# Optimization experiments

Hardware: AMD Instinct MI355X
Metric: run time of the kernel (lower is better)

## Reference

```python
import jax, jax.numpy as jnp
import numpy as np

N_NODES = 100000
N_EDGES = 1600000
D_IN = 128
D_OUT = 128


def setup_inputs() -> dict:
    key = jax.random.key(0)
    k1, k2, k3, k4, k5 = jax.random.split(key, 5)
    features = jax.random.normal(k1, (N_NODES, D_IN), dtype=jnp.float32)
    edge_row = jax.random.randint(k2, (N_EDGES,), 0, N_NODES, dtype=jnp.int32)
    edge_col = jax.random.randint(k3, (N_EDGES,), 0, N_NODES, dtype=jnp.int32)
    edge_val = jax.random.uniform(k4, (N_EDGES,), dtype=jnp.float32)
    # Xavier-uniform weight, zero bias, ones skip weight (matches reset_parameters)
    limit = float(np.sqrt(6.0 / (D_IN + D_OUT)))
    weight = jax.random.uniform(k5, (D_IN, D_OUT), minval=-limit, maxval=limit, dtype=jnp.float32)
    bias = jnp.zeros((D_OUT,), dtype=jnp.float32)
    skip_weight = jnp.ones((D_OUT,), dtype=jnp.float32)
    return {"features": features, "edge_row": edge_row, "edge_col": edge_col,
            "edge_val": edge_val, "weight": weight, "bias": bias,
            "skip_weight": skip_weight}


def reference(features, edge_row, edge_col, edge_val, weight, bias, skip_weight):
    # Dense projection: [N, Din] @ [Din, Dout] -> [N, Dout]
    h = features @ weight
    # SpMM in COO form: Ah[r] = sum_e val[e] * h[col[e]] for edges with row[e]==r
    gathered = edge_val[:, None] * h[edge_col]          # [E, Dout]
    Ah = jax.ops.segment_sum(gathered, edge_row, num_segments=N_NODES)
    # Skip-scale + bias + activation epilogue
    out = h * skip_weight[None, :] + Ah + bias[None, :]
    return jax.nn.selu(out)
```

## Files before the change

kernel.cpp:

```cpp
#include <hip/hip_runtime.h>

#define N_NODES 100000
#define N_EDGES 1600000
#define D 128
#define BM 64
#define GEMM_BLKS 1563

#define BROWS 128
#define NB 782
#define EB 250
#define EPB 6400
#define NTAB (NB * EB)
#define SCAN_BLKS 191

typedef __attribute__((ext_vector_type(8))) short short8_t;
typedef __attribute__((ext_vector_type(4))) float float4_t;

__device__ __forceinline__ unsigned pack_bf16x2(float a, float b) {
    unsigned ua = __float_as_uint(a);
    unsigned ub = __float_as_uint(b);
    ua = (ua + 0x7fffu + ((ua >> 16) & 1u)) >> 16;
    ub = (ub + 0x7fffu + ((ub >> 16) & 1u)) & 0xffff0000u;
    return ua | ub;
}

__device__ __forceinline__ float selu_f(float x) {
    const float SCALE = 1.0507009873554805f;
    const float ALPHA = 1.6732632423543772f;
    return x > 0.f ? SCALE * x : SCALE * ALPHA * (expf(x) - 1.f);
}

__global__ __launch_bounds__(256) void bhist_prep_kernel(
    const int* __restrict__ erow, const float* __restrict__ W,
    unsigned* __restrict__ tbl, unsigned short* __restrict__ wt)
{
    __shared__ unsigned hcnt[NB];
    const int t = threadIdx.x;
    if (blockIdx.x < EB) {
        const int k = blockIdx.x;
        for (int i = t; i < NB; i += 256) hcnt[i] = 0;
        __syncthreads();
        const int4* q = (const int4*)(erow + k * EPB);
        for (int i = t; i < EPB / 4; i += 256) {
            const int4 r = q[i];
            atomicAdd(&hcnt[r.x >> 7], 1u);
            atomicAdd(&hcnt[r.y >> 7], 1u);
            atomicAdd(&hcnt[r.z >> 7], 1u);
            atomicAdd(&hcnt[r.w >> 7], 1u);
        }
        __syncthreads();
        for (int i = t; i < NB; i += 256) tbl[k * NB + i] = hcnt[i];
    } else {
        const int pb = blockIdx.x - EB;
        for (int idx = pb * 4096 + t; idx < (pb + 1) * 4096; idx += 256) {
            const int k = idx >> 7, n = idx & 127;
            unsigned u = __float_as_uint(W[idx]);
            u = (u + 0x7fffu + ((u >> 16) & 1u)) >> 16;
            wt[n * D + k] = (unsigned short)u;
        }
    }
}

__global__ __launch_bounds__(1024) void scan_local_kernel(
    const unsigned* __restrict__ tbl, unsigned* __restrict__ lex,
    unsigned* __restrict__ bsum)
{
    __shared__ unsigned wsum[16];
    const int t = threadIdx.x;
    const int L = blockIdx.x * 1024 + t;
    const int lane = t & 63;

    unsigned v = 0;
    if (L < NTAB) {
        const int b = L / EB;
        const int k = L - b * EB;
        v = tbl[k * NB + b];
    }
    unsigned x = v;
#pragma unroll
    for (int d = 1; d < 64; d <<= 1) {
        const unsigned y = __shfl_up(x, d, 64);
        if (lane >= d) x += y;
    }
    if (lane == 63) wsum[t >> 6] = x;
    __syncthreads();
    unsigned add = 0;
    for (int w = 0; w < (t >> 6); ++w) add += wsum[w];
    x += add;
    if (L < NTAB) lex[L] = x - v;
    if (t == 1023) bsum[blockIdx.x] = x;
}

__global__ __launch_bounds__(256) void scan_blk_kernel(unsigned* __restrict__ bsum)
{
    __shared__ unsigned ws[4];
    const int t = threadIdx.x, lane = t & 63, w = t >> 6;
    unsigned v = (t < SCAN_BLKS) ? bsum[t] : 0u;
    unsigned x = v;
#pragma unroll
    for (int d = 1; d < 64; d <<= 1) {
        const unsigned y = __shfl_up(x, d, 64);
        if (lane >= d) x += y;
    }
    if (lane == 63) ws[w] = x;
    __syncthreads();
    unsigned add = 0;
    for (int i = 0; i < w; ++i) add += ws[i];
    x += add;
    if (t < SCAN_BLKS) bsum[t] = x - v;
}

__global__ __launch_bounds__(1024) void scan_apply_kernel(
    const unsigned* __restrict__ lex, const unsigned* __restrict__ boff,
    unsigned* __restrict__ tbl)
{
    const int L = blockIdx.x * 1024 + threadIdx.x;
    if (L >= NTAB) return;
    const int b = L / EB;
    const int k = L - b * EB;
    tbl[k * NB + b] = lex[L] + boff[blockIdx.x];
}

__global__ __launch_bounds__(256) void gemm_scatter_kernel(
    const float* __restrict__ feat, const unsigned short* __restrict__ wt,
    unsigned* __restrict__ h16,
    const int* __restrict__ erow, const int* __restrict__ ecol,
    const float* __restrict__ eval_, const unsigned* __restrict__ tbl,
    int2* __restrict__ rec)
{
    __shared__ __align__(16) char smem[52224];
    const int t = threadIdx.x;

    if (blockIdx.x < GEMM_BLKS) {
        short* At = (short*)smem;
        short* Wt = (short*)(smem + 17408);
        const int rowBase = blockIdx.x * BM;

        {
            const int n = t >> 1, hf = t & 1;
            const uint4* src = (const uint4*)(wt + n * D + hf * 64);
            uint4* dst = (uint4*)&Wt[n * 136 + hf * 64];
#pragma unroll
            for (int j = 0; j < 8; ++j) dst[j] = src[j];
        }
        {
#pragma unroll
            for (int i = 0; i < 8; ++i) {
                const int p = t + 256 * i;
                const int r = p >> 5, kq = p & 31;
                int row = rowBase + r;
                if (row >= N_NODES) row = N_NODES - 1;
                const float4 f = *(const float4*)&feat[(size_t)row * D + kq * 4];
                uint2 u;
                u.x = pack_bf16x2(f.x, f.y);
                u.y = pack_bf16x2(f.z, f.w);
                *(uint2*)&At[r * 136 + kq * 4] = u;
            }
        }
        __syncthreads();

        const int w = t >> 6, lane = t & 63;
        const int m16 = lane & 15, kg = lane >> 4;

        short8_t a_frag[4];
        const int arow = w * 16 + m16;
#pragma unroll
        for (int k0 = 0; k0 < 4; ++k0)
            a_frag[k0] = *(const short8_t*)&At[arow * 136 + k0 * 32 + kg * 8];

#pragma unroll
        for (int nt = 0; nt < 8; ++nt) {
            float4_t acc = {0.f, 0.f, 0.f, 0.f};
#pragma unroll
            for (int k0 = 0; k0 < 4; ++k0) {
                const short8_t b =
                    *(const short8_t*)&Wt[(nt * 16 + m16) * 136 + k0 * 32 + kg * 8];
                acc = __builtin_amdgcn_mfma_f32_16x16x32_bf16(a_frag[k0], b, acc, 0, 0, 0);
            }
            float mine[4], part[4];
#pragma unroll
            for (int i = 0; i < 4; ++i) {
                mine[i] = acc[i];
                part[i] = __shfl_xor(mine[i], 1, 64);
            }
            if ((m16 & 1) == 0) {
                const int cp = (nt * 16 + m16) >> 1;
#pragma unroll
                for (int i = 0; i < 4; ++i) {
                    const int row = rowBase + w * 16 + kg * 4 + i;
                    if (row < N_NODES)
                        h16[(size_t)row * 64 + cp] = pack_bf16x2(mine[i], part[i]);
                }
            }
        }
    } else {
        unsigned* rk = (unsigned*)smem;
        const int k = blockIdx.x - GEMM_BLKS;
        for (int i = t; i < NB; i += 256) rk[i] = 0;
        __syncthreads();

        const int4*   qr = (const int4*)(erow + k * EPB);
        const int4*   qc = (const int4*)(ecol + k * EPB);
        const float4* qv = (const float4*)(eval_ + k * EPB);
        const unsigned* base = tbl + k * NB;

        for (int i = t; i < EPB / 4; i += 256) {
            const int4   r = qr[i];
            const int4   c = qc[i];
            const float4 v = qv[i];
            {
                const int b = r.x >> 7;
                const unsigned pos = base[b] + atomicAdd(&rk[b], 1u);
                rec[pos] = make_int2(c.x | ((r.x & 127) << 17), __float_as_int(v.x));
            }
            {
                const int b = r.y >> 7;
                const unsigned pos = base[b] + atomicAdd(&rk[b], 1u);
                rec[pos] = make_int2(c.y | ((r.y & 127) << 17), __float_as_int(v.y));
            }
            {
                const int b = r.z >> 7;
                const unsigned pos = base[b] + atomicAdd(&rk[b], 1u);
                rec[pos] = make_int2(c.z | ((r.z & 127) << 17), __float_as_int(v.z));
            }
            {
                const int b = r.w >> 7;
                const unsigned pos = base[b] + atomicAdd(&rk[b], 1u);
                rec[pos] = make_int2(c.w | ((r.w & 127) << 17), __float_as_int(v.w));
            }
        }
    }
}

__global__ __launch_bounds__(256) void bsort_kernel(
    const unsigned* __restrict__ tbl, const int2* __restrict__ rec,
    int2* __restrict__ rec2, unsigned* __restrict__ rstart)
{
    __shared__ unsigned cnt[BROWS], base[BROWS], rk[BROWS];
    __shared__ unsigned w0tot;
    const int t = threadIdx.x, b = blockIdx.x;
    if (t < BROWS) { cnt[t] = 0; rk[t] = 0; }
    __syncthreads();

    const unsigned s = tbl[b];
    const unsigned e = (b == NB - 1) ? N_EDGES : tbl[b + 1];

    for (unsigned j = s + t; j < e; j += 256)
        atomicAdd(&cnt[(rec[j].x >> 17) & 127], 1u);
    __syncthreads();

    unsigned v = 0, x = 0;
    if (t < BROWS) {
        v = cnt[t]; x = v;
#pragma unroll
        for (int d = 1; d < 64; d <<= 1) {
            const unsigned y = __shfl_up(x, d, 64);
            if ((t & 63) >= d) x += y;
        }
    }
    if (t == 63) w0tot = x;
    __syncthreads();
    if (t < BROWS) {
        const unsigned ex = x - v + ((t >= 64) ? w0tot : 0u);
        base[t] = s + ex;
        const int row = b * BROWS + t;
        if (row < N_NODES) rstart[row] = s + ex;
    }
    __syncthreads();

    for (unsigned j = s + t; j < e; j += 256) {
        const int2 R = rec[j];
        const int rl = (R.x >> 17) & 127;
        const unsigned pos = base[rl] + atomicAdd(&rk[rl], 1u);
        rec2[pos] = R;
    }
}

__global__ __launch_bounds__(256) void spmm_csr_kernel(
    const unsigned* __restrict__ rstart, const int2* __restrict__ rec,
    const unsigned* __restrict__ h16, const float* __restrict__ skip,
    const float* __restrict__ bias, float* __restrict__ out)
{
    const int row = blockIdx.x * 4 + (threadIdx.x >> 6);
    if (row >= N_NODES) return;
    const int lane = threadIdx.x & 63;
    const int half = lane >> 5, sub = lane & 31;

    const unsigned s = rstart[row];
    const unsigned e = (row == N_NODES - 1) ? N_EDGES : rstart[row + 1];

    const uint2* h2 = (const uint2*)h16;

    float4 a0 = make_float4(0.f, 0.f, 0.f, 0.f);
    float4 a1 = a0, a2 = a0, a3 = a0;

    for (unsigned j = s; j < e; j += 16) {
        int2  R[8];
        uint2 p[8];
        float v[8];
#pragma unroll
        for (int k = 0; k < 8; ++k) {
            const unsigned jj = j + 2 * k + half;
            const unsigned ji = jj < e ? jj : e - 1;
            R[k] = rec[ji];
            v[k] = (jj < e) ? __int_as_float(R[k].y) : 0.f;
        }
#pragma unroll
        for (int k = 0; k < 8; ++k)
            p[k] = h2[(size_t)(R[k].x & 0x1FFFF) * 32 + sub];

#pragma unroll
        for (int k = 0; k < 8; ++k) {
            float4* a = (k & 3) == 0 ? &a0 : (k & 3) == 1 ? &a1 : (k & 3) == 2 ? &a2 : &a3;
            a->x += v[k] * __uint_as_float(p[k].x << 16);
            a->y += v[k] * __uint_as_float(p[k].x & 0xffff0000u);
            a->z += v[k] * __uint_as_float(p[k].y << 16);
            a->w += v[k] * __uint_as_float(p[k].y & 0xffff0000u);
        }
    }

    float4 a;
    a.x = (a0.x + a1.x) + (a2.x + a3.x);
    a.y = (a0.y + a1.y) + (a2.y + a3.y);
    a.z = (a0.z + a1.z) + (a2.z + a3.z);
    a.w = (a0.w + a1.w) + (a2.w + a3.w);
    a.x += __shfl_xor(a.x, 32, 64);
    a.y += __shfl_xor(a.y, 32, 64);
    a.z += __shfl_xor(a.z, 32, 64);
    a.w += __shfl_xor(a.w, 32, 64);

    if (half == 0) {
        const int c4 = sub * 4;
        const uint2 hp = h2[(size_t)row * 32 + sub];
        const float4 sk = *(const float4*)&skip[c4];
        const float4 bs = *(const float4*)&bias[c4];
        float4 o;
        o.x = __uint_as_float(hp.x << 16) * sk.x + bs.x + a.x;
        o.y = __uint_as_float(hp.x & 0xffff0000u) * sk.y + bs.y + a.y;
        o.z = __uint_as_float(hp.y << 16) * sk.z + bs.z + a.z;
        o.w = __uint_as_float(hp.y & 0xffff0000u) * sk.w + bs.w + a.w;
        o.x = selu_f(o.x); o.y = selu_f(o.y); o.z = selu_f(o.z); o.w = selu_f(o.w);
        *(float4*)&out[(size_t)row * D + c4] = o;
    }
}

__global__ __launch_bounds__(256) void gemm_fb_kernel(
    const float* __restrict__ feat, const float* __restrict__ W,
    const float* __restrict__ bias, const float* __restrict__ skip,
    float* __restrict__ h, float* __restrict__ out)
{
    __shared__ float Wl[D * D];
    __shared__ float Fl[32 * D];
    const int tid = threadIdx.x;

    const float4* W4 = (const float4*)W;
    float4* Wl4 = (float4*)Wl;
#pragma unroll
    for (int i = 0; i < 16; ++i) Wl4[tid + 256 * i] = W4[tid + 256 * i];

    const size_t rowBase = (size_t)blockIdx.x * 32;
    const float4* F4 = (const float4*)(feat + rowBase * D);
    float4* Fl4 = (float4*)Fl;
#pragma unroll
    for (int i = 0; i < 4; ++i) Fl4[tid + 256 * i] = F4[tid + 256 * i];
    __syncthreads();

    const int colg = (tid & 31) * 4;
    const int row0 = (tid >> 5) * 4;
    float4 acc[4];
#pragma unroll
    for (int r = 0; r < 4; ++r) acc[r] = make_float4(0.f, 0.f, 0.f, 0.f);
#pragma unroll 4
    for (int k = 0; k < D; ++k) {
        const float4 w = *(const float4*)&Wl[k * D + colg];
#pragma unroll
        for (int r = 0; r < 4; ++r) {
            const float aa = Fl[(row0 + r) * D + k];
            acc[r].x += aa * w.x; acc[r].y += aa * w.y;
            acc[r].z += aa * w.z; acc[r].w += aa * w.w;
        }
    }
    const float4 sk = *(const float4*)&skip[colg];
    const float4 bs = *(const float4*)&bias[colg];
#pragma unroll
    for (int r = 0; r < 4; ++r) {
        const size_t row = rowBase + row0 + r;
        *(float4*)&h[row * D + colg] = acc[r];
        float4 o;
        o.x = acc[r].x * sk.x + bs.x; o.y = acc[r].y * sk.y + bs.y;
        o.z = acc[r].z * sk.z + bs.z; o.w = acc[r].w * sk.w + bs.w;
        *(float4*)&out[row * D + colg] = o;
    }
}

__global__ __launch_bounds__(256) void spmm_atomic_kernel(
    const int* __restrict__ erow, const int* __restrict__ ecol,
    const float* __restrict__ eval_, const float* __restrict__ h,
    float* __restrict__ out)
{
    const int e = blockIdx.x * 4 + (threadIdx.x >> 6);
    if (e >= N_EDGES) return;
    const int lane = threadIdx.x & 63;
    const int r = erow[e];
    const int c = ecol[e];
    const float v = eval_[e];
    const float2 hv = *(const float2*)&h[(size_t)c * D + lane * 2];
    float* o = &out[(size_t)r * D + lane * 2];
    atomicAdd(o + 0, v * hv.x);
    atomicAdd(o + 1, v * hv.y);
}

__global__ __launch_bounds__(256) void selu_kernel(float* __restrict__ out)
{
    const size_t i = (size_t)blockIdx.x * blockDim.x + threadIdx.x;
    float4 v = ((float4*)out)[i];
    v.x = selu_f(v.x); v.y = selu_f(v.y); v.z = selu_f(v.z); v.w = selu_f(v.w);
    ((float4*)out)[i] = v;
}

extern "C" void kernel_launch(void* const* d_in, const int* in_sizes, int n_in,
                              void* d_out, int out_size, void* d_ws, size_t ws_size,
                              hipStream_t stream)
{
    const float* feat  = (const float*)d_in[0];
    const int*   erow  = (const int*)d_in[1];
    const int*   ecol  = (const int*)d_in[2];
    const float* eval_ = (const float*)d_in[3];
    const float* W     = (const float*)d_in[4];
    const float* bias  = (const float*)d_in[5];
    const float* skip  = (const float*)d_in[6];

    float* out = (float*)d_out;

    const size_t off_h16  = 0;
    const size_t off_tbl  = 25600000;
    const size_t off_lex  = 26382000;
    const size_t off_bs   = 27164336;
    const size_t off_rst  = 27165360;
    const size_t off_wt   = 27565360;
    const size_t off_rec  = 27598128;
    const size_t off_rec2 = 40398128;
    const size_t needed   = 53198128;

    char* ws = (char*)d_ws;
    unsigned*       h16    = (unsigned*)(ws + off_h16);
    unsigned*       tbl    = (unsigned*)(ws + off_tbl);
    unsigned*       lex    = (unsigned*)(ws + off_lex);
    unsigned*       bsum   = (unsigned*)(ws + off_bs);
    unsigned*       rstart = (unsigned*)(ws + off_rst);
    unsigned short* wt     = (unsigned short*)(ws + off_wt);
    int2*           rec    = (int2*)(ws + off_rec);
    int2*           rec2   = (int2*)(ws + off_rec2);

    if (ws_size >= needed) {
        bhist_prep_kernel<<<EB + 4, 256, 0, stream>>>(erow, W, tbl, wt);
        scan_local_kernel<<<SCAN_BLKS, 1024, 0, stream>>>(tbl, lex, bsum);
        scan_blk_kernel<<<1, 256, 0, stream>>>(bsum);
        scan_apply_kernel<<<SCAN_BLKS, 1024, 0, stream>>>(lex, bsum, tbl);
        gemm_scatter_kernel<<<GEMM_BLKS + EB, 256, 0, stream>>>(
            feat, wt, h16, erow, ecol, eval_, tbl, rec);
        bsort_kernel<<<NB, 256, 0, stream>>>(tbl, rec, rec2, rstart);
        spmm_csr_kernel<<<(N_NODES + 3) / 4, 256, 0, stream>>>(
            rstart, rec2, h16, skip, bias, out);
    } else {
        float* h = (float*)d_ws;
        gemm_fb_kernel<<<N_NODES / 32, 256, 0, stream>>>(feat, W, bias, skip, h, out);
        spmm_atomic_kernel<<<N_EDGES / 4, 256, 0, stream>>>(erow, ecol, eval_, h, out);
        selu_kernel<<<(N_NODES * D) / (256 * 4), 256, 0, stream>>>(out);
    }
}
```

Measured before the change: 138.7 us.

## Remap CSR SpMM to one wave per four rows with full-row lanes

The CSR SpMM kernel now gives each 64-lane wave four consecutive rows. Every lane owns two columns of a full 256-byte bf16 row, where before the wave split edges into two half-waves of 32 lanes with four columns each. Row bounds are loaded once per wave and made uniform with readfirstlane, and the cross-half shuffle reduction is removed. The aim is to cut per-row setup and reduction overhead and issue wider coalesced gathers. In exchange, the wave now walks four rows one after another, so there is less memory-level parallelism per wave and row-length imbalance can build up.

```diff
diff --git a/kernel.cpp b/kernel.cpp
--- a/kernel.cpp
+++ b/kernel.cpp
@@ -12,6 +12,8 @@
 #define EPB 6400
 #define NTAB (NB * EB)
 #define SCAN_BLKS 191
+
+#define SPMM_BLKS 6250
 
 typedef __attribute__((ext_vector_type(8))) short short8_t;
 typedef __attribute__((ext_vector_type(4))) float float4_t;
@@ -281,66 +283,65 @@
     const unsigned* __restrict__ h16, const float* __restrict__ skip,
     const float* __restrict__ bias, float* __restrict__ out)
 {
-    const int row = blockIdx.x * 4 + (threadIdx.x >> 6);
-    if (row >= N_NODES) return;
     const int lane = threadIdx.x & 63;
-    const int half = lane >> 5, sub = lane & 31;
-
-    const unsigned s = rstart[row];
-    const unsigned e = (row == N_NODES - 1) ? N_EDGES : rstart[row + 1];
-
-    const uint2* h2 = (const uint2*)h16;
-
-    float4 a0 = make_float4(0.f, 0.f, 0.f, 0.f);
-    float4 a1 = a0, a2 = a0, a3 = a0;
-
-    for (unsigned j = s; j < e; j += 16) {
-        int2  R[8];
-        uint2 p[8];
-        float v[8];
-#pragma unroll
-        for (int k = 0; k < 8; ++k) {
-            const unsigned jj = j + 2 * k + half;
-            const unsigned ji = jj < e ? jj : e - 1;
-            R[k] = rec[ji];
-            v[k] = (jj < e) ? __int_as_float(R[k].y) : 0.f;
-        }
-#pragma unroll
-        for (int k = 0; k < 8; ++k)
-            p[k] = h2[(size_t)(R[k].x & 0x1FFFF) * 32 + sub];
-
-#pragma unroll
-        for (int k = 0; k < 8; ++k) {
-            float4* a = (k & 3) == 0 ? &a0 : (k & 3) == 1 ? &a1 : (k & 3) == 2 ? &a2 : &a3;
-            a->x += v[k] * __uint_as_float(p[k].x << 16);
-            a->y += v[k] * __uint_as_float(p[k].x & 0xffff0000u);
-            a->z += v[k] * __uint_as_float(p[k].y << 16);
-            a->w += v[k] * __uint_as_float(p[k].y & 0xffff0000u);
-        }
-    }
-
-    float4 a;
-    a.x = (a0.x + a1.x) + (a2.x + a3.x);
-    a.y = (a0.y + a1.y) + (a2.y + a3.y);
-    a.z = (a0.z + a1.z) + (a2.z + a3.z);
-    a.w = (a0.w + a1.w) + (a2.w + a3.w);
-    a.x += __shfl_xor(a.x, 32, 64);
-    a.y += __shfl_xor(a.y, 32, 64);
-    a.z += __shfl_xor(a.z, 32, 64);
-    a.w += __shfl_xor(a.w, 32, 64);
-
-    if (half == 0) {
-        const int c4 = sub * 4;
-        const uint2 hp = h2[(size_t)row * 32 + sub];
-        const float4 sk = *(const float4*)&skip[c4];
-        const float4 bs = *(const float4*)&bias[c4];
-        float4 o;
-        o.x = __uint_as_float(hp.x << 16) * sk.x + bs.x + a.x;
-        o.y = __uint_as_float(hp.x & 0xffff0000u) * sk.y + bs.y + a.y;
-        o.z = __uint_as_float(hp.y << 16) * sk.z + bs.z + a.z;
-        o.w = __uint_as_float(hp.y & 0xffff0000u) * sk.w + bs.w + a.w;
-        o.x = selu_f(o.x); o.y = selu_f(o.y); o.z = selu_f(o.z); o.w = selu_f(o.w);
-        *(float4*)&out[(size_t)row * D + c4] = o;
+    const int wid  = threadIdx.x >> 6;
+    const int rowBase = (blockIdx.x * 4 + wid) * 4;
+
+    const int c2 = lane * 2;
+    const float2 sk = *(const float2*)&skip[c2];
+    const float2 bs = *(const float2*)&bias[c2];
+
+    unsigned sb[5];
+#pragma unroll
+    for (int i = 0; i < 5; ++i) {
+        const int rr = rowBase + i;
+        const unsigned bnd = (rr < N_NODES) ? rstart[rr] : (unsigned)N_EDGES;
+        sb[i] = (unsigned)__builtin_amdgcn_readfirstlane((int)bnd);
+    }
+
+#pragma unroll
+    for (int r = 0; r < 4; ++r) {
+        const int row = rowBase + r;
+        const unsigned s = sb[r];
+        const unsigned e = sb[r + 1];
+
+        float ax = 0.f, ay = 0.f, bx = 0.f, by = 0.f;
+
+        for (unsigned j = s; j < e; j += 8) {
+            int2     E[8];
+            unsigned valid[8];
+#pragma unroll
+            for (int k = 0; k < 8; ++k) {
+                const unsigned idx = j + (unsigned)k;
+                const unsigned ji  = idx < e ? idx : e - 1u;
+                E[k] = rec[ji];
+                valid[k] = (idx < e) ? 1u : 0u;
+            }
+            unsigned g[8];
+#pragma unroll
+            for (int k = 0; k < 8; ++k) {
+                const unsigned node = ((unsigned)E[k].x) & 0x1FFFFu;
+                g[k] = h16[(size_t)node * 64 + lane];
+            }
+#pragma unroll
+            for (int k = 0; k < 8; ++k) {
+                const float v = valid[k] ? __int_as_float(E[k].y) : 0.f;
+                float* px = (k & 1) ? &bx : &ax;
+                float* py = (k & 1) ? &by : &ay;
+                *px = fmaf(v, __uint_as_float(g[k] << 16), *px);
+                *py = fmaf(v, __uint_as_float(g[k] & 0xffff0000u), *py);
+            }
+        }
+
+        const unsigned hw = h16[(size_t)row * 64 + lane];
+        float ox = fmaf(__uint_as_float(hw << 16),         sk.x, (ax + bx) + bs.x);
+        float oy = fmaf(__uint_as_float(hw & 0xffff0000u), sk.y, (ay + by) + bs.y);
+        ox = selu_f(ox);
+        oy = selu_f(oy);
+        float2 o;
+        o.x = ox;
+        o.y = oy;
+        *(float2*)&out[(size_t)row * D + c2] = o;
     }
 }
 
@@ -460,7 +461,7 @@
         gemm_scatter_kernel<<<GEMM_BLKS + EB, 256, 0, stream>>>(
             feat, wt, h16, erow, ecol, eval_, tbl, rec);
         bsort_kernel<<<NB, 256, 0, stream>>>(tbl, rec, rec2, rstart);
-        spmm_csr_kernel<<<(N_NODES + 3) / 4, 256, 0, stream>>>(
+        spmm_csr_kernel<<<SPMM_BLKS, 256, 0, stream>>>(
             rstart, rec2, h16, skip, bias, out);
     } else {
         float* h = (float*)d_ws;
```

After: 135.9 us. 2.0% less time.
